# Kernel optimization log

Measured on AMD Instinct MI355X. Metric: run time of the kernel, lower is better.

## Reference

```python
import jax, jax.numpy as jnp
import numpy as np

L, H, C, DH, FF = 6, 8, 512, 64, 2048
B, T, S = 64, 128, 128
EPS = 1e-5


def setup_inputs() -> dict:
    key = jax.random.key(0)
    ks = jax.random.split(key, 20)
    sc = 0.02
    def w(k, shape):
        return jax.random.normal(k, shape, dtype=jnp.float32) * sc
    inp = {
        "x": jax.random.normal(ks[0], (B, T, C), dtype=jnp.float32),
        "encoder_output": jax.random.normal(ks[1], (B, S, C), dtype=jnp.float32),
        # per-head self-attention projections, stacked over layers and heads
        "sa_wq": w(ks[2], (L, H, C, DH)), "sa_bq": w(ks[3], (L, H, DH)),
        "sa_wk": w(ks[4], (L, H, C, DH)), "sa_bk": w(ks[5], (L, H, DH)),
        "sa_wv": w(ks[6], (L, H, C, DH)), "sa_bv": w(ks[7], (L, H, DH)),
        # per-head cross-attention projections
        "ca_wq": w(ks[8], (L, H, C, DH)), "ca_bq": w(ks[9], (L, H, DH)),
        "ca_wk": w(ks[10], (L, H, C, DH)), "ca_bk": w(ks[11], (L, H, DH)),
        "ca_wv": w(ks[12], (L, H, C, DH)), "ca_bv": w(ks[13], (L, H, DH)),
        # feed-forward
        "ff_w1": w(ks[14], (L, C, FF)), "ff_b1": w(ks[15], (L, FF)),
        "ff_w2": w(ks[16], (L, FF, C)), "ff_b2": w(ks[17], (L, C)),
    }
    return inp


def _layer_norm_2d(x):
    # F.layer_norm(x, (T, C)): normalize jointly over last two dims, no affine
    mu = jnp.mean(x, axis=(1, 2), keepdims=True)
    var = jnp.var(x, axis=(1, 2), keepdims=True)
    return (x - mu) * jax.lax.rsqrt(var + EPS)


def _mha(qx, kvx, wq, bq, wk, bk, wv, bv):
    # wq/wk/wv: [H, C, DH]; per-head projections, vectorized over heads.
    q = jnp.einsum("btc,hcd->bhtd", qx, wq) + bq[:, None, :]
    k = jnp.einsum("bsc,hcd->bhsd", kvx, wk) + bk[:, None, :]
    v = jnp.einsum("bsc,hcd->bhsd", kvx, wv) + bv[:, None, :]
    scores = jax.nn.softmax(jnp.einsum("bhtd,bhsd->bhts", q, k) * (DH ** -0.5), axis=-1)
    out = jnp.einsum("bhts,bhsd->bhtd", scores, v)
    b, h, t, d = out.shape  # concat heads along feature dim
    return out.transpose(0, 2, 1, 3).reshape(b, t, h * d)


def reference(x, encoder_output, sa_wq, sa_bq, sa_wk, sa_bk, sa_wv, sa_bv,
              ca_wq, ca_bq, ca_wk, ca_bk, ca_wv, ca_bv,
              ff_w1, ff_b1, ff_w2, ff_b2):
    for l in range(L):
        # masked MHA (note: original code never applies the causal mask)
        x = x + _mha(x, x, sa_wq[l], sa_bq[l], sa_wk[l], sa_bk[l], sa_wv[l], sa_bv[l])
        x = _layer_norm_2d(x)
        # cross attention: q from decoder, k/v from encoder output
        x = x + _mha(x, encoder_output, ca_wq[l], ca_bq[l], ca_wk[l], ca_bk[l], ca_wv[l], ca_bv[l])
        x = _layer_norm_2d(x)
        # feed-forward
        h = jax.nn.relu(jnp.einsum("btc,cf->btf", x, ff_w1[l]) + ff_b1[l])
        x = x + (jnp.einsum("btf,fc->btc", h, ff_w2[l]) + ff_b2[l])
        x = _layer_norm_2d(x)
    return x
```

## Files before the change

### kernel.cpp

```cpp
#include <hip/hip_runtime.h>
#include <hip/hip_bf16.h>


typedef __bf16 bf16;
typedef bf16 bf16x8 __attribute__((ext_vector_type(8)));
typedef float f32x4 __attribute__((ext_vector_type(4)));

#define MFMA16(a, b, c) __builtin_amdgcn_mfma_f32_16x16x32_bf16(a, b, c, 0, 0, 0)

#define GLL16(gsrc, ldst)                                                          \
    __builtin_amdgcn_global_load_lds(                                              \
        (const __attribute__((address_space(1))) void*)(gsrc),                     \
        (__attribute__((address_space(3))) void*)(ldst), 16, 0, 0)

static constexpr int L_ = 6, C_ = 512, FF_ = 2048;
static constexpr int B_ = 64, T_ = 128;
static constexpr int M_ = B_ * T_;
static constexpr float LNINV = 1.f / 65536.f;
static constexpr float EPS_ = 1e-5f;

__global__ __launch_bounds__(256) void zero_part(float* __restrict__ p) {
    for (int i = threadIdx.x; i < 18 * 64 * 2; i += 256) p[i] = 0.f;
}

__global__ __launch_bounds__(256) void init_x(
    const float* __restrict__ xin, float* __restrict__ y, bf16* __restrict__ yb)
{
    const size_t i = ((size_t)blockIdx.x * 256 + threadIdx.x) * 8;
    float4 f0 = *(const float4*)(xin + i);
    float4 f1 = *(const float4*)(xin + i + 4);
    *(float4*)(y + i) = f0;
    *(float4*)(y + i + 4) = f1;
    bf16x8 v = {(bf16)f0.x, (bf16)f0.y, (bf16)f0.z, (bf16)f0.w,
                (bf16)f1.x, (bf16)f1.y, (bf16)f1.z, (bf16)f1.w};
    *(bf16x8*)(yb + i) = v;
}

__global__ __launch_bounds__(256) void to_bf16(
    const float* __restrict__ in, bf16* __restrict__ out)
{
    const size_t i = ((size_t)blockIdx.x * 256 + threadIdx.x) * 8;
    float4 f0 = *(const float4*)(in + i);
    float4 f1 = *(const float4*)(in + i + 4);
    bf16x8 v = {(bf16)f0.x, (bf16)f0.y, (bf16)f0.z, (bf16)f0.w,
                (bf16)f1.x, (bf16)f1.y, (bf16)f1.z, (bf16)f1.w};
    *(bf16x8*)(out + i) = v;
}

__global__ __launch_bounds__(256) void transpose_f32_bf16(
    const float* __restrict__ src, bf16* __restrict__ dst, int R, int C)
{
    __shared__ alignas(16) float t[64][68];
    const int r0 = blockIdx.y * 64, c0 = blockIdx.x * 64;
    const int tr = threadIdx.x >> 4;
    const int tc = (threadIdx.x & 15) * 4;
#pragma unroll
    for (int ro = 0; ro < 64; ro += 16)
        *(float4*)&t[tr + ro][tc] = *(const float4*)(src + (size_t)(r0 + tr + ro) * C + c0 + tc);
    __syncthreads();
    const int wc = (threadIdx.x & 7) * 8;
#pragma unroll
    for (int po = 0; po < 2; ++po) {
        const int oc = (threadIdx.x >> 3) + po * 32;
        bf16x8 v;
#pragma unroll
        for (int j = 0; j < 8; ++j) v[j] = (bf16)t[wc + j][oc];
        *(bf16x8*)(dst + (size_t)(c0 + oc) * R + r0 + wc) = v;
    }
}

__global__ __launch_bounds__(256) void head_repack(
    const float* __restrict__ sa_wq, const float* __restrict__ sa_wk,
    const float* __restrict__ sa_wv, const float* __restrict__ ca_wq,
    const float* __restrict__ ca_wk, const float* __restrict__ ca_wv,
    bf16* __restrict__ Wsa, bf16* __restrict__ Wcaq, bf16* __restrict__ Wcakv)
{
    __shared__ alignas(16) float t[64][68];
    const int z = blockIdx.z;
    const int type = z / 48, rem = z % 48, l = rem >> 3, h = rem & 7;
    const float* srcs[6] = {sa_wq, sa_wk, sa_wv, ca_wq, ca_wk, ca_wv};
    const float* s = srcs[type] + (size_t)(l * 8 + h) * 512 * 64;
    bf16* d;
    if (type < 3)       d = Wsa   + ((size_t)l * 1536 + type * 512 + h * 64) * 512;
    else if (type == 3) d = Wcaq  + ((size_t)l * 512 + h * 64) * 512;
    else                d = Wcakv + ((size_t)l * 1024 + (type - 4) * 512 + h * 64) * 512;
    const int r0 = blockIdx.y * 64;
    const int tr = threadIdx.x >> 4;
    const int tc = (threadIdx.x & 15) * 4;
#pragma unroll
    for (int ro = 0; ro < 64; ro += 16)
        *(float4*)&t[tr + ro][tc] = *(const float4*)(s + (size_t)(r0 + tr + ro) * 64 + tc);
    __syncthreads();
    const int wc = (threadIdx.x & 7) * 8;
#pragma unroll
    for (int po = 0; po < 2; ++po) {
        const int oc = (threadIdx.x >> 3) + po * 32;
        bf16x8 v;
#pragma unroll
        for (int j = 0; j < 8; ++j) v[j] = (bf16)t[wc + j][oc];
        *(bf16x8*)(d + (size_t)oc * 512 + r0 + wc) = v;
    }
}

__global__ __launch_bounds__(256) void colsum_all(
    const float* __restrict__ sa_wq, const float* __restrict__ sa_wk,
    const float* __restrict__ sa_wv, const float* __restrict__ ca_wq,
    const float* __restrict__ ff_w1,
    float* __restrict__ csA, float* __restrict__ csQ, float* __restrict__ csF)
{
    const int t = blockIdx.x * 256 + threadIdx.x;
    const int l = t >> 12, u = t & 4095;
    float sum = 0.f;
    if (u < 1536) {
        const int p = u >> 9, h = (u >> 6) & 7, d = u & 63;
        const float* w = (p == 0) ? sa_wq : (p == 1) ? sa_wk : sa_wv;
        const float* base = w + (size_t)(l * 8 + h) * 512 * 64 + d;
        for (int c = 0; c < 512; ++c) sum += base[(size_t)c * 64];
        csA[l * 1536 + u] = sum;
    } else if (u < 2048) {
        const int v = u - 1536, h = v >> 6, d = v & 63;
        const float* base = ca_wq + (size_t)(l * 8 + h) * 512 * 64 + d;
        for (int c = 0; c < 512; ++c) sum += base[(size_t)c * 64];
        csQ[l * 512 + v] = sum;
    } else {
        const int f = u - 2048;
        const float* base = ff_w1 + (size_t)l * 512 * 2048 + f;
        for (int c = 0; c < 512; ++c) sum += base[(size_t)c * 2048];
        csF[l * 2048 + f] = sum;
    }
}

template <int MODE, int BM>
__global__ __launch_bounds__(512) void gemm_bt(
    const bf16* __restrict__ A, const bf16* __restrict__ BT,
    const float* __restrict__ b0, const float* __restrict__ b1,
    const float* __restrict__ b2, const float* __restrict__ cs,
    float2* __restrict__ part, int slotPrev, int slotNew,
    bf16* __restrict__ o0, bf16* __restrict__ o1, bf16* __restrict__ o2,
    float* __restrict__ y, bf16* __restrict__ ybf, int N, int K)
{
    constexpr int MI = (BM == 128) ? 4 : 2;
    constexpr int NI = 2;
    constexpr int AR = BM / 8;
    constexpr int AGLL = BM / 64;
    constexpr int VG = AGLL + 2;
    __shared__ alignas(16) bf16 as[2][BM][64];
    __shared__ alignas(16) bf16 bs[2][128][64];
    const int tid = threadIdx.x, wave = tid >> 6, lane = tid & 63;

    const int gx = gridDim.x;
    int wgid = blockIdx.y * gx + blockIdx.x;
    {
        const int nwg = gx * gridDim.y;
        const int q = nwg >> 3, r = nwg & 7;
        const int xcd = wgid & 7, idx = wgid >> 3;
        wgid = (xcd < r ? xcd * (q + 1) : r * (q + 1) + (xcd - r) * q) + idx;
    }
    const int m0 = (wgid / gx) * BM, n0 = (wgid % gx) * 128;

    const int wr = (wave >> 2) * (BM / 2);
    const int wc = (wave & 3) * 32;
    const int fr = lane & 15, fq = lane >> 4;
    const int xr = fr & 7;

    float mu = 0.f, rstd = 1.f;
    if (slotPrev >= 0) {
        float2 p = part[slotPrev * 64 + (m0 >> 7)];
        mu = p.x * LNINV;
        rstd = rsqrtf(p.y * LNINV - mu * mu + EPS_);
    }

    const int rlane = lane >> 3;
    const int scol = ((lane & 7) ^ rlane) * 8;
    const bf16* pa = A + (size_t)(m0 + wave * AR + rlane) * K + scol;
    const bf16* pb = BT + (size_t)(n0 + wave * 16 + rlane) * K + scol;

    auto stage = [&](int buf, int k0) {
#pragma unroll
        for (int i = 0; i < AGLL; ++i)
            GLL16(pa + k0 + (size_t)(8 * i) * K, &as[buf][wave * AR + 8 * i][0]);
#pragma unroll
        for (int i = 0; i < 2; ++i)
            GLL16(pb + k0 + (size_t)(8 * i) * K, &bs[buf][wave * 16 + 8 * i][0]);
    };

    f32x4 acc[MI][NI] = {};
    bf16x8 af[MI], bfv[NI];
    auto frags = [&](int buf, int kk) {
#pragma unroll
        for (int mi = 0; mi < MI; ++mi)
            af[mi] = *(const bf16x8*)&as[buf][wr + mi * 16 + fr][(((kk << 2) + fq) ^ xr) << 3];
#pragma unroll
        for (int ni = 0; ni < NI; ++ni)
            bfv[ni] = *(const bf16x8*)&bs[buf][wc + ni * 16 + fr][(((kk << 2) + fq) ^ xr) << 3];
    };
    auto cluster = [&]() {
        __builtin_amdgcn_s_setprio(1);
#pragma unroll
        for (int mi = 0; mi < MI; ++mi)
#pragma unroll
            for (int ni = 0; ni < NI; ++ni)
                acc[mi][ni] = MFMA16(af[mi], bfv[ni], acc[mi][ni]);
        __builtin_amdgcn_s_setprio(0);
    };

    const int nt = K >> 6;
    stage(0, 0);
    stage(1, 64);

    int cur = 0;
    for (int t = 0; t < nt - 1; ++t) {
        asm volatile("s_waitcnt vmcnt(%0)\n\ts_barrier" :: "n"(VG) : "memory");
        frags(cur, 0);
        asm volatile("s_waitcnt lgkmcnt(0)" ::: "memory");
        __builtin_amdgcn_sched_barrier(0);
        cluster();
        frags(cur, 1);
        asm volatile("s_waitcnt lgkmcnt(0)" ::: "memory");
        __builtin_amdgcn_sched_barrier(0);
        __builtin_amdgcn_s_barrier();
        if (t + 2 < nt) stage(cur, (t + 2) << 6);
        cluster();
        cur ^= 1;
    }
    asm volatile("s_waitcnt vmcnt(0)\n\ts_barrier" ::: "memory");
    frags(cur, 0);
    asm volatile("s_waitcnt lgkmcnt(0)" ::: "memory");
    __builtin_amdgcn_sched_barrier(0);
    cluster();
    frags(cur, 1);
    asm volatile("s_waitcnt lgkmcnt(0)" ::: "memory");
    __builtin_amdgcn_sched_barrier(0);
    cluster();

    float s = 0.f, ss = 0.f;
    const float murs = mu * rstd;
#pragma unroll
    for (int mi = 0; mi < MI; ++mi) {
#pragma unroll
        for (int ni = 0; ni < NI; ++ni) {
            const int n = n0 + wc + ni * 16 + fr;
#pragma unroll
            for (int reg = 0; reg < 4; ++reg) {
                const int r = m0 + wr + mi * 16 + fq * 4 + reg;
                float val = acc[mi][ni][reg];
                if constexpr (MODE == 0) {
                    const int p = n >> 9, hd = n & 511, d = n & 63, hh = (n >> 6) & 7;
                    const int bb = r >> 7, tt = r & 127;
                    const float* bias = (p == 0) ? b0 : (p == 1 ? b1 : b2);
                    val = val * rstd + bias[hd] - murs * cs[n];
                    const size_t bh = (size_t)(bb * 8 + hh);
                    if (p == 0)      o0[(bh * 128 + tt) * 64 + d] = (bf16)val;
                    else if (p == 1) o1[(bh * 128 + tt) * 64 + d] = (bf16)val;
                    else             o2[(bh * 64 + d) * 128 + tt] = (bf16)val;
                } else if constexpr (MODE == 1) {
                    const int d = n & 63, hh = (n >> 6) & 7;
                    const int bb = r >> 7, tt = r & 127;
                    val = val * rstd + b0[n] - murs * cs[n];
                    o0[((size_t)(bb * 8 + hh) * 128 + tt) * 64 + d] = (bf16)val;
                } else if constexpr (MODE == 2) {
                    const int p = n >> 9, hd = n & 511, d = n & 63, hh = (n >> 6) & 7;
                    const int bb = r >> 7, tt = r & 127;
                    val += (p == 0) ? b1[hd] : b2[hd];
                    const size_t bh = (size_t)(bb * 8 + hh);
                    if (p == 0) o1[(bh * 128 + tt) * 64 + d] = (bf16)val;
                    else        o2[(bh * 64 + d) * 128 + tt] = (bf16)val;
                } else if constexpr (MODE == 3) {
                    val = val * rstd + b0[n] - murs * cs[n];
                    val = fmaxf(val, 0.f);
                    o0[(size_t)r * 2048 + n] = (bf16)val;
                } else {
                    const size_t idx = (size_t)r * 512 + n;
                    const float v = (y[idx] - mu) * rstd + val + b0[n];
                    y[idx] = v;
                    ybf[idx] = (bf16)v;
                    s += v;
                    ss += v * v;
                }
            }
        }
    }
    if constexpr (MODE == 4) {
        for (int off = 32; off; off >>= 1) { s += __shfl_xor(s, off); ss += __shfl_xor(ss, off); }
        __shared__ float rs[8], rss[8];
        if (lane == 0) { rs[wave] = s; rss[wave] = ss; }
        __syncthreads();
        if (tid == 0) {
            float sa = 0.f, sb = 0.f;
#pragma unroll
            for (int w = 0; w < 8; ++w) { sa += rs[w]; sb += rss[w]; }
            float2* dst = &part[slotNew * 64 + (m0 >> 7)];
            atomicAdd(&dst->x, sa);
            atomicAdd(&dst->y, sb);
        }
    }
}

__global__ __launch_bounds__(256) void attn_kernel(
    const bf16* __restrict__ q, const bf16* __restrict__ k,
    const bf16* __restrict__ vT, float* __restrict__ y, bf16* __restrict__ ybf,
    float2* __restrict__ part, int slotPrev, int slotNew)
{
    __shared__ alignas(16) bf16 sP[128][136];
    __shared__ float sPart[2][128];
    const int bh = blockIdx.x;
    const int bb = bh >> 3, hh = bh & 7;
    const bf16* Q = q + (size_t)bh * 128 * 64;
    const bf16* Kp = k + (size_t)bh * 128 * 64;
    const bf16* V = vT + (size_t)bh * 64 * 128;
    const int tid = threadIdx.x, wave = tid >> 6, lane = tid & 63;
    const int wr = (wave >> 1) * 64, wc = (wave & 1) * 64;
    const int fr = lane & 15, fq = lane >> 4;

    float mu = 0.f, rstd = 1.f;
    if (slotPrev >= 0) {
        float2 p = part[slotPrev * 64 + bb];
        mu = p.x * LNINV;
        rstd = rsqrtf(p.y * LNINV - mu * mu + EPS_);
    }

    f32x4 acc[4][4] = {};
#pragma unroll
    for (int k0 = 0; k0 < 64; k0 += 32) {
        bf16x8 af[4], bfv[4];
#pragma unroll
        for (int mi = 0; mi < 4; ++mi)
            af[mi] = *(const bf16x8*)(Q + (size_t)(wr + mi * 16 + fr) * 64 + k0 + fq * 8);
#pragma unroll
        for (int ni = 0; ni < 4; ++ni)
            bfv[ni] = *(const bf16x8*)(Kp + (size_t)(wc + ni * 16 + fr) * 64 + k0 + fq * 8);
#pragma unroll
        for (int mi = 0; mi < 4; ++mi)
#pragma unroll
            for (int ni = 0; ni < 4; ++ni)
                acc[mi][ni] = MFMA16(af[mi], bfv[ni], acc[mi][ni]);
    }

    const int colw = wave & 1;
#pragma unroll
    for (int mi = 0; mi < 4; ++mi) {
#pragma unroll
        for (int reg = 0; reg < 4; ++reg) {
            const int r = wr + mi * 16 + fq * 4 + reg;
            float rsum = 0.f;
#pragma unroll
            for (int ni = 0; ni < 4; ++ni) {
                const float e = __expf(acc[mi][ni][reg] * 0.125f);
                sP[r][wc + ni * 16 + fr] = (bf16)e;
                rsum += e;
            }
            rsum += __shfl_xor(rsum, 1);
            rsum += __shfl_xor(rsum, 2);
            rsum += __shfl_xor(rsum, 4);
            rsum += __shfl_xor(rsum, 8);
            if (fr == 0) sPart[colw][r] = rsum;
        }
    }
    __syncthreads();

    f32x4 acc2[2][4] = {};
#pragma unroll
    for (int k0 = 0; k0 < 128; k0 += 32) {
        bf16x8 af[2], bfv[4];
#pragma unroll
        for (int mi = 0; mi < 2; ++mi)
            af[mi] = *(const bf16x8*)&sP[wave * 32 + mi * 16 + fr][k0 + fq * 8];
#pragma unroll
        for (int ni = 0; ni < 4; ++ni)
            bfv[ni] = *(const bf16x8*)(V + (size_t)(ni * 16 + fr) * 128 + k0 + fq * 8);
#pragma unroll
        for (int mi = 0; mi < 2; ++mi)
#pragma unroll
            for (int ni = 0; ni < 4; ++ni)
                acc2[mi][ni] = MFMA16(af[mi], bfv[ni], acc2[mi][ni]);
    }

    float inv[2][4];
#pragma unroll
    for (int mi = 0; mi < 2; ++mi)
#pragma unroll
        for (int reg = 0; reg < 4; ++reg) {
            const int r = wave * 32 + mi * 16 + fq * 4 + reg;
            inv[mi][reg] = 1.f / (sPart[0][r] + sPart[1][r]);
        }

    float s = 0.f, ss = 0.f;
#pragma unroll
    for (int mi = 0; mi < 2; ++mi)
#pragma unroll
        for (int ni = 0; ni < 4; ++ni)
#pragma unroll
            for (int reg = 0; reg < 4; ++reg) {
                const int r = wave * 32 + mi * 16 + fq * 4 + reg;
                const int d = ni * 16 + fr;
                const size_t idx = ((size_t)(bb * 128 + r)) * 512 + hh * 64 + d;
                const float v = (y[idx] - mu) * rstd + acc2[mi][ni][reg] * inv[mi][reg];
                y[idx] = v;
                ybf[idx] = (bf16)v;
                s += v;
                ss += v * v;
            }
    for (int off = 32; off; off >>= 1) { s += __shfl_xor(s, off); ss += __shfl_xor(ss, off); }
    __shared__ float rs[4], rss[4];
    if (lane == 0) { rs[wave] = s; rss[wave] = ss; }
    __syncthreads();
    if (tid == 0) {
        float2* dst = &part[slotNew * 64 + bb];
        atomicAdd(&dst->x, rs[0] + rs[1] + rs[2] + rs[3]);
        atomicAdd(&dst->y, rss[0] + rss[1] + rss[2] + rss[3]);
    }
}

__global__ __launch_bounds__(256) void final_norm(
    const float* __restrict__ y, const float2* __restrict__ part, int slot,
    float* __restrict__ out)
{
    const size_t i = ((size_t)blockIdx.x * 256 + threadIdx.x) * 4;
    const int b = (int)(i >> 16);
    float2 p = part[slot * 64 + b];
    const float mu = p.x * LNINV;
    const float rstd = rsqrtf(p.y * LNINV - mu * mu + EPS_);
    float4 v = *(const float4*)(y + i);
    float4 o = {(v.x - mu) * rstd, (v.y - mu) * rstd, (v.z - mu) * rstd, (v.w - mu) * rstd};
    *(float4*)(out + i) = o;
}

extern "C" void kernel_launch(void* const* d_in, const int* in_sizes, int n_in,
                              void* d_out, int out_size, void* d_ws, size_t ws_size,
                              hipStream_t stream)
{
    (void)in_sizes; (void)n_in; (void)out_size; (void)ws_size;
    const float* x_in  = (const float*)d_in[0];
    const float* enc   = (const float*)d_in[1];
    const float* sa_wq = (const float*)d_in[2];
    const float* sa_bq = (const float*)d_in[3];
    const float* sa_wk = (const float*)d_in[4];
    const float* sa_bk = (const float*)d_in[5];
    const float* sa_wv = (const float*)d_in[6];
    const float* sa_bv = (const float*)d_in[7];
    const float* ca_wq = (const float*)d_in[8];
    const float* ca_bq = (const float*)d_in[9];
    const float* ca_wk = (const float*)d_in[10];
    const float* ca_bk = (const float*)d_in[11];
    const float* ca_wv = (const float*)d_in[12];
    const float* ca_bv = (const float*)d_in[13];
    const float* ff_w1 = (const float*)d_in[14];
    const float* ff_b1 = (const float*)d_in[15];
    const float* ff_w2 = (const float*)d_in[16];
    const float* ff_b2 = (const float*)d_in[17];

    char* wsp = (char*)d_ws;
    auto alloc = [&](size_t bytes) -> char* {
        char* p = wsp;
        wsp += (bytes + 255) & ~(size_t)255;
        return p;
    };
    float* y     = (float*)alloc((size_t)M_ * 512 * 4);
    bf16*  ybf   = (bf16*)alloc((size_t)M_ * 512 * 2);
    bf16*  encbf = (bf16*)alloc((size_t)M_ * 512 * 2);
    char*  shreg = alloc((size_t)M_ * 2048 * 2);
    bf16*  WsaA  = (bf16*)alloc((size_t)L_ * 1536 * 512 * 2);
    bf16*  WcaqA = (bf16*)alloc((size_t)L_ * 512 * 512 * 2);
    bf16*  WcakvA= (bf16*)alloc((size_t)L_ * 1024 * 512 * 2);
    bf16*  Wff1  = (bf16*)alloc((size_t)2048 * 512 * 2);
    bf16*  Wff2  = (bf16*)alloc((size_t)512 * 2048 * 2);
    float* csA   = (float*)alloc((size_t)L_ * 1536 * 4);
    float* csQ   = (float*)alloc((size_t)L_ * 512 * 4);
    float* csF   = (float*)alloc((size_t)L_ * 2048 * 4);
    float2* part = (float2*)alloc(18 * 64 * sizeof(float2));

    bf16* qb   = (bf16*)shreg;
    bf16* kb   = (bf16*)(shreg + (size_t)512 * 128 * 64 * 2);
    bf16* vTb  = (bf16*)(shreg + (size_t)2 * 512 * 128 * 64 * 2);
    bf16* hbuf = (bf16*)shreg;

    dim3 tb(256), tbg(512);
    zero_part<<<1, tb, 0, stream>>>((float*)part);
    init_x<<<2048, tb, 0, stream>>>(x_in, y, ybf);
    to_bf16<<<2048, tb, 0, stream>>>(enc, encbf);
    head_repack<<<dim3(1, 8, 288), tb, 0, stream>>>(sa_wq, sa_wk, sa_wv, ca_wq, ca_wk, ca_wv,
                                                    WsaA, WcaqA, WcakvA);
    colsum_all<<<96, tb, 0, stream>>>(sa_wq, sa_wk, sa_wv, ca_wq, ff_w1, csA, csQ, csF);

    for (int l = 0; l < L_; ++l) {
        transpose_f32_bf16<<<dim3(32, 8, 1), tb, 0, stream>>>(ff_w1 + (size_t)l * 512 * 2048, Wff1, 512, 2048);
        transpose_f32_bf16<<<dim3(8, 32, 1), tb, 0, stream>>>(ff_w2 + (size_t)l * 2048 * 512, Wff2, 2048, 512);
        const int sPrev = (l == 0) ? -1 : (l - 1) * 3 + 2;
        gemm_bt<0, 128><<<dim3(12, 64), tbg, 0, stream>>>(ybf, WsaA + (size_t)l * 1536 * 512,
            sa_bq + l * 512, sa_bk + l * 512, sa_bv + l * 512, csA + l * 1536,
            part, sPrev, -1, qb, kb, vTb, nullptr, nullptr, 1536, 512);
        attn_kernel<<<512, tb, 0, stream>>>(qb, kb, vTb, y, ybf, part, sPrev, l * 3 + 0);
        gemm_bt<1, 64><<<dim3(4, 128), tbg, 0, stream>>>(ybf, WcaqA + (size_t)l * 512 * 512,
            ca_bq + l * 512, nullptr, nullptr, csQ + l * 512,
            part, l * 3 + 0, -1, qb, nullptr, nullptr, nullptr, nullptr, 512, 512);
        gemm_bt<2, 128><<<dim3(8, 64), tbg, 0, stream>>>(encbf, WcakvA + (size_t)l * 1024 * 512,
            nullptr, ca_bk + l * 512, ca_bv + l * 512, nullptr,
            part, -1, -1, nullptr, kb, vTb, nullptr, nullptr, 1024, 512);
        attn_kernel<<<512, tb, 0, stream>>>(qb, kb, vTb, y, ybf, part, l * 3 + 0, l * 3 + 1);
        gemm_bt<3, 128><<<dim3(16, 64), tbg, 0, stream>>>(ybf, Wff1,
            ff_b1 + l * 2048, nullptr, nullptr, csF + l * 2048,
            part, l * 3 + 1, -1, hbuf, nullptr, nullptr, nullptr, nullptr, 2048, 512);
        gemm_bt<4, 64><<<dim3(4, 128), tbg, 0, stream>>>(hbuf, Wff2,
            ff_b2 + l * 512, nullptr, nullptr, nullptr,
            part, l * 3 + 1, l * 3 + 2, nullptr, nullptr, nullptr, y, ybf, 512, 2048);
    }
    final_norm<<<4096, tb, 0, stream>>>(y, part, 17, (float*)d_out);
}
```

Baseline: 1.338 ms.

## Double GEMM row tiles and split column-sum reduction across blocks with atomics

Raises the GEMM M tile: the larger GEMMs move from 128 to 256 rows and the smaller ones from 64 to 128. Wave layout changes to a 4x2 arrangement with more N fragments per wave for the 256 case, and the per-wave layernorm stats index is now computed from each wave's row offset. Separately, the weight column-sum precompute is split over 8 row chunks with atomicAdd into zeroed buffers, which adds parallelism to that setup kernel. The larger tiles raise register and LDS pressure and halve the number of workgroups, which risks occupancy and load balance.

Result: slower. 1.400 ms (+4.7%).

```diff
diff --git a/kernel.cpp b/kernel.cpp
--- a/kernel.cpp
+++ b/kernel.cpp
@@ -19,8 +19,15 @@
 static constexpr float LNINV = 1.f / 65536.f;
 static constexpr float EPS_ = 1e-5f;
 
-__global__ __launch_bounds__(256) void zero_part(float* __restrict__ p) {
-    for (int i = threadIdx.x; i < 18 * 64 * 2; i += 256) p[i] = 0.f;
+__global__ __launch_bounds__(256) void zero_all(
+    float* __restrict__ csA, float* __restrict__ csQ, float* __restrict__ csF,
+    float* __restrict__ part)
+{
+    const int i = blockIdx.x * 256 + threadIdx.x;
+    if (i < 6 * 1536) csA[i] = 0.f;
+    if (i < 6 * 512)  csQ[i] = 0.f;
+    if (i < 6 * 2048) csF[i] = 0.f;
+    if (i < 18 * 64 * 2) part[i] = 0.f;
 }
 
 __global__ __launch_bounds__(256) void init_x(
@@ -110,24 +117,38 @@
 {
     const int t = blockIdx.x * 256 + threadIdx.x;
     const int l = t >> 12, u = t & 4095;
-    float sum = 0.f;
+    const int r0 = blockIdx.y * 64;
+    const float* base;
+    int stride;
+    float* out;
     if (u < 1536) {
         const int p = u >> 9, h = (u >> 6) & 7, d = u & 63;
         const float* w = (p == 0) ? sa_wq : (p == 1) ? sa_wk : sa_wv;
-        const float* base = w + (size_t)(l * 8 + h) * 512 * 64 + d;
-        for (int c = 0; c < 512; ++c) sum += base[(size_t)c * 64];
-        csA[l * 1536 + u] = sum;
+        base = w + (size_t)(l * 8 + h) * 512 * 64 + d;
+        stride = 64;
+        out = &csA[l * 1536 + u];
     } else if (u < 2048) {
         const int v = u - 1536, h = v >> 6, d = v & 63;
-        const float* base = ca_wq + (size_t)(l * 8 + h) * 512 * 64 + d;
-        for (int c = 0; c < 512; ++c) sum += base[(size_t)c * 64];
-        csQ[l * 512 + v] = sum;
+        base = ca_wq + (size_t)(l * 8 + h) * 512 * 64 + d;
+        stride = 64;
+        out = &csQ[l * 512 + v];
     } else {
         const int f = u - 2048;
-        const float* base = ff_w1 + (size_t)l * 512 * 2048 + f;
-        for (int c = 0; c < 512; ++c) sum += base[(size_t)c * 2048];
-        csF[l * 2048 + f] = sum;
-    }
+        base = ff_w1 + (size_t)l * 512 * 2048 + f;
+        stride = 2048;
+        out = &csF[l * 2048 + f];
+    }
+    const float* p = base + (size_t)r0 * stride;
+    float s0 = 0.f, s1 = 0.f, s2 = 0.f, s3 = 0.f;
+#pragma unroll 4
+    for (int c = 0; c < 64; c += 4) {
+        s0 += p[0];
+        s1 += p[(size_t)stride];
+        s2 += p[(size_t)2 * stride];
+        s3 += p[(size_t)3 * stride];
+        p += (size_t)4 * stride;
+    }
+    atomicAdd(out, (s0 + s1) + (s2 + s3));
 }
 
 template <int MODE, int BM>
@@ -139,8 +160,9 @@
     bf16* __restrict__ o0, bf16* __restrict__ o1, bf16* __restrict__ o2,
     float* __restrict__ y, bf16* __restrict__ ybf, int N, int K)
 {
-    constexpr int MI = (BM == 128) ? 4 : 2;
-    constexpr int NI = 2;
+    constexpr int WC = (BM == 256) ? 2 : 4;
+    constexpr int MI = 4;
+    constexpr int NI = (BM == 256) ? 4 : 2;
     constexpr int AR = BM / 8;
     constexpr int AGLL = BM / 64;
     constexpr int VG = AGLL + 2;
@@ -158,14 +180,14 @@
     }
     const int m0 = (wgid / gx) * BM, n0 = (wgid % gx) * 128;
 
-    const int wr = (wave >> 2) * (BM / 2);
-    const int wc = (wave & 3) * 32;
+    const int wr = ((WC == 2) ? (wave >> 1) : (wave >> 2)) * 64;
+    const int wc = (wave & (WC - 1)) * (128 / WC);
     const int fr = lane & 15, fq = lane >> 4;
     const int xr = fr & 7;
 
     float mu = 0.f, rstd = 1.f;
     if (slotPrev >= 0) {
-        float2 p = part[slotPrev * 64 + (m0 >> 7)];
+        float2 p = part[slotPrev * 64 + ((m0 + wr) >> 7)];
         mu = p.x * LNINV;
         rstd = rsqrtf(p.y * LNINV - mu * mu + EPS_);
     }
@@ -475,32 +497,32 @@
     bf16* hbuf = (bf16*)shreg;
 
     dim3 tb(256), tbg(512);
-    zero_part<<<1, tb, 0, stream>>>((float*)part);
+    zero_all<<<48, tb, 0, stream>>>(csA, csQ, csF, (float*)part);
     init_x<<<2048, tb, 0, stream>>>(x_in, y, ybf);
     to_bf16<<<2048, tb, 0, stream>>>(enc, encbf);
     head_repack<<<dim3(1, 8, 288), tb, 0, stream>>>(sa_wq, sa_wk, sa_wv, ca_wq, ca_wk, ca_wv,
                                                     WsaA, WcaqA, WcakvA);
-    colsum_all<<<96, tb, 0, stream>>>(sa_wq, sa_wk, sa_wv, ca_wq, ff_w1, csA, csQ, csF);
+    colsum_all<<<dim3(96, 8), tb, 0, stream>>>(sa_wq, sa_wk, sa_wv, ca_wq, ff_w1, csA, csQ, csF);
 
     for (int l = 0; l < L_; ++l) {
         transpose_f32_bf16<<<dim3(32, 8, 1), tb, 0, stream>>>(ff_w1 + (size_t)l * 512 * 2048, Wff1, 512, 2048);
         transpose_f32_bf16<<<dim3(8, 32, 1), tb, 0, stream>>>(ff_w2 + (size_t)l * 2048 * 512, Wff2, 2048, 512);
         const int sPrev = (l == 0) ? -1 : (l - 1) * 3 + 2;
-        gemm_bt<0, 128><<<dim3(12, 64), tbg, 0, stream>>>(ybf, WsaA + (size_t)l * 1536 * 512,
+        gemm_bt<0, 256><<<dim3(12, 32), tbg, 0, stream>>>(ybf, WsaA + (size_t)l * 1536 * 512,
             sa_bq + l * 512, sa_bk + l * 512, sa_bv + l * 512, csA + l * 1536,
             part, sPrev, -1, qb, kb, vTb, nullptr, nullptr, 1536, 512);
         attn_kernel<<<512, tb, 0, stream>>>(qb, kb, vTb, y, ybf, part, sPrev, l * 3 + 0);
-        gemm_bt<1, 64><<<dim3(4, 128), tbg, 0, stream>>>(ybf, WcaqA + (size_t)l * 512 * 512,
+        gemm_bt<1, 128><<<dim3(4, 64), tbg, 0, stream>>>(ybf, WcaqA + (size_t)l * 512 * 512,
             ca_bq + l * 512, nullptr, nullptr, csQ + l * 512,
             part, l * 3 + 0, -1, qb, nullptr, nullptr, nullptr, nullptr, 512, 512);
-        gemm_bt<2, 128><<<dim3(8, 64), tbg, 0, stream>>>(encbf, WcakvA + (size_t)l * 1024 * 512,
+        gemm_bt<2, 256><<<dim3(8, 32), tbg, 0, stream>>>(encbf, WcakvA + (size_t)l * 1024 * 512,
             nullptr, ca_bk + l * 512, ca_bv + l * 512, nullptr,
             part, -1, -1, nullptr, kb, vTb, nullptr, nullptr, 1024, 512);
         attn_kernel<<<512, tb, 0, stream>>>(qb, kb, vTb, y, ybf, part, l * 3 + 0, l * 3 + 1);
-        gemm_bt<3, 128><<<dim3(16, 64), tbg, 0, stream>>>(ybf, Wff1,
+        gemm_bt<3, 256><<<dim3(16, 32), tbg, 0, stream>>>(ybf, Wff1,
             ff_b1 + l * 2048, nullptr, nullptr, csF + l * 2048,
             part, l * 3 + 1, -1, hbuf, nullptr, nullptr, nullptr, nullptr, 2048, 512);
-        gemm_bt<4, 64><<<dim3(4, 128), tbg, 0, stream>>>(hbuf, Wff2,
+        gemm_bt<4, 128><<<dim3(4, 64), tbg, 0, stream>>>(hbuf, Wff2,
             ff_b2 + l * 512, nullptr, nullptr, nullptr,
             part, l * 3 + 1, l * 3 + 2, nullptr, nullptr, nullptr, y, ybf, 512, 2048);
     }
```
